# Kernel tuning notes

Measured on AMD Instinct MI355X. Metric: run time of the kernel, lower is better.

Reference implementation:

```python
import jax, jax.numpy as jnp
import numpy as np

B, H, W = 16, 512, 512
N_BINS = 511          # round(mean(shape)) - 1 for (512, 512)
MAX_R = 1.0           # (1 + min(shape)/max(shape)) / 2 for square image


def _bin_ids():
    # Precompute per-pixel radial shell index (replaces the list of boolean shell masks).
    frame = max(H, W)
    xx, yy = np.mgrid[:H, :W]
    ellipse = ((xx - H / 2) * 2 / frame) ** 2 + ((yy - W / 2) * 2 / frame) ** 2
    r2 = np.linspace(0.0, MAX_R, N_BINS + 1)[1:] ** 2
    # shell k = { r2[k-1] <= ellipse < r2[k] }; pixels with ellipse >= r2[-1] map to
    # overflow bin N_BINS and are dropped, exactly matching the xor'd ellipse masks.
    return jnp.asarray(np.searchsorted(r2, ellipse.ravel(), side='right').astype(np.int32))


BIN_IDS = _bin_ids()  # [H*W] int32 in [0, N_BINS]


def setup_inputs() -> dict:
    key = jax.random.key(0)
    k1, k2 = jax.random.split(key)
    return {
        "z_": jax.random.normal(k1, (B, H, W, 2), dtype=jnp.float32),
        "t_": jax.random.normal(k2, (B, H, W, 2), dtype=jnp.float32),
    }


def _shell_sums(x):
    # x: [B, H*W] -> per-shell sums [B, N_BINS+1] in a single fused segment-sum pass.
    return jax.vmap(lambda v: jax.ops.segment_sum(v, BIN_IDS, num_segments=N_BINS + 1))(x)


def reference(z_, t_):
    tc = t_[..., 0] + 1j * t_[..., 1]          # [B,H,W] complex target
    zc = z_[..., 0] + 1j * z_[..., 1]
    Ft = jnp.fft.fft2(tc, axes=(-2, -1))
    Fe = jnp.fft.fft2(zc - tc, axes=(-2, -1))
    norm_coeff = Ft.real ** 2 + Ft.imag ** 2   # |FFT(target)|^2, [B,H,W]
    errors = Fe.real ** 2 + Fe.imag ** 2       # |FFT(z - target)|^2
    es = _shell_sums(errors.reshape(B, -1))[:, :N_BINS]      # drop overflow bin
    ns = _shell_sums(norm_coeff.reshape(B, -1))[:, :N_BINS]
    nre = es / jnp.maximum(ns, 1e-8)           # per-batch, per-shell normed error
    # per_shell_loss = per-batch sum over shells; loss = mean over batch
    return jnp.mean(jnp.sum(nre, axis=1))
```

## Files before the change

### kernel.cpp

```cpp
#include <hip/hip_runtime.h>

#define HH 512
#define WW 512
#define NBATCH 16
#define NBINS 512

#define PI_F 3.14159265358979323846f

#define SW(r) ((r) ^ (((r) >> 4) & 0xF))
#define TSW(c, hh) (((c) << 3) + ((hh) ^ (((c) >> 1) & 7)))

#define DPP_SHR(x, n) __builtin_amdgcn_update_dpp(0, (x), 0x110 + (n), 0xF, 0xF, true)
#define DPP_SHL1(x)   __builtin_amdgcn_update_dpp(0, (x), 0x101,       0xF, 0xF, true)

__device__ __forceinline__ float2 cadd(float2 a, float2 b){ return make_float2(a.x+b.x, a.y+b.y); }
__device__ __forceinline__ float2 csub(float2 a, float2 b){ return make_float2(a.x-b.x, a.y-b.y); }
__device__ __forceinline__ float2 cmul(float2 a, float2 b){
    return make_float2(a.x*b.x - a.y*b.y, a.x*b.y + a.y*b.x);
}

__device__ __forceinline__ void dft8(const float2* a, float2* y) {
    const float s2 = 0.70710678118654752440f;
    float2 t02a = cadd(a[0], a[4]), t02s = csub(a[0], a[4]);
    float2 t13a = cadd(a[2], a[6]), t13s = csub(a[2], a[6]);
    float2 E0 = cadd(t02a, t13a);
    float2 E2 = csub(t02a, t13a);
    float2 E1 = make_float2(t02s.x + t13s.y, t02s.y - t13s.x);
    float2 E3 = make_float2(t02s.x - t13s.y, t02s.y + t13s.x);
    float2 u02a = cadd(a[1], a[5]), u02s = csub(a[1], a[5]);
    float2 u13a = cadd(a[3], a[7]), u13s = csub(a[3], a[7]);
    float2 O0 = cadd(u02a, u13a);
    float2 O2 = csub(u02a, u13a);
    float2 O1 = make_float2(u02s.x + u13s.y, u02s.y - u13s.x);
    float2 O3 = make_float2(u02s.x - u13s.y, u02s.y + u13s.x);
    float2 wO1 = make_float2(s2 * (O1.x + O1.y), s2 * (O1.y - O1.x));
    float2 wO2 = make_float2(O2.y, -O2.x);
    float2 wO3 = make_float2(s2 * (O3.y - O3.x), -s2 * (O3.x + O3.y));
    y[0] = cadd(E0, O0);  y[4] = csub(E0, O0);
    y[1] = cadd(E1, wO1); y[5] = csub(E1, wO1);
    y[2] = cadd(E2, wO2); y[6] = csub(E2, wO2);
    y[3] = cadd(E3, wO3); y[7] = csub(E3, wO3);
}

__device__ __forceinline__ void twiddle8(float base, float2* w) {
    float s1, c1, s4, c4;
    __sincosf(base, &s1, &c1);
    __sincosf(4.0f * base, &s4, &c4);
    w[0] = make_float2(1.0f, 0.0f);
    w[1] = make_float2(c1, s1);
    w[2] = cmul(w[1], w[1]);
    w[3] = cmul(w[2], w[1]);
    w[4] = make_float2(c4, s4);
    w[5] = cmul(w[4], w[1]);
    w[6] = cmul(w[4], w[2]);
    w[7] = cmul(w[4], w[3]);
}

__device__ __forceinline__ void fft512_stage0_store(float2* rb, int lane, const float2* a) {
    float2 y[8]; dft8(a, y);
    float2 w[8]; twiddle8(-PI_F * (float)lane * (1.0f / 256.0f), w);
#pragma unroll
    for (int r = 0; r < 8; ++r) rb[SW(8 * lane + r)] = cmul(y[r], w[r]);
}

__device__ __forceinline__ void fft512_stage1(float2* rb, int lane) {
    float2 a[8];
#pragma unroll
    for (int u = 0; u < 8; ++u) a[u] = rb[SW(lane + 64 * u)];
    float2 y[8]; dft8(a, y);
    float2 w[8]; twiddle8(-PI_F * (float)(lane >> 3) * (1.0f / 32.0f), w);
    const int qb = (lane & 7) + ((lane >> 3) << 6);
#pragma unroll
    for (int r = 0; r < 8; ++r) rb[SW(qb + 8 * r)] = cmul(y[r], w[r]);
}

__device__ __forceinline__ void fft512_stage2(const float2* rb, int lane, float2* y) {
    float2 a[8];
#pragma unroll
    for (int u = 0; u < 8; ++u) a[u] = rb[SW(lane + 64 * u)];
    dft8(a, y);
}

__global__ __launch_bounds__(512, 4)
void row_fft_kernel(const float2* __restrict__ z, const float2* __restrict__ t,
                    float2* __restrict__ fieldsT, int b0) {
    __shared__ float2 buf[8 * 512];
    const int tid  = threadIdx.x;
    const int lane = tid & 63;
    const int g    = tid >> 6;
    const int bid  = blockIdx.x;
    const int hg   = bid & 63;
    const int lb   = bid >> 6;
    const int b    = b0 + lb;
    const int h    = (hg << 3) | g;
    const size_t rowOff = ((size_t)(b * HH + h)) * WW;

    const float2* tr = t + rowOff;
    const float2* zr = z + rowOff;
    float2 tv[8], zv[8];
#pragma unroll
    for (int u = 0; u < 8; ++u) tv[u] = tr[lane + 64 * u];
#pragma unroll
    for (int u = 0; u < 8; ++u) zv[u] = zr[lane + 64 * u];

    float2* rb = buf + (g << 9);
#pragma unroll
    for (int f = 0; f < 2; ++f) {
        float2 a[8];
        if (f == 0) {
#pragma unroll
            for (int u = 0; u < 8; ++u) a[u] = tv[u];
        } else {
#pragma unroll
            for (int u = 0; u < 8; ++u) a[u] = make_float2(zv[u].x - tv[u].x,
                                                           zv[u].y - tv[u].y);
        }
        fft512_stage0_store(rb, lane, a);
        __builtin_amdgcn_wave_barrier();
        fft512_stage1(rb, lane);
        __builtin_amdgcn_wave_barrier();
        float2 y[8];
        fft512_stage2(rb, lane, y);

        __syncthreads();
#pragma unroll
        for (int r = 0; r < 8; ++r) {
            int c = lane + (r << 6);
            buf[TSW(c, g)] = y[r];
        }
        __syncthreads();
        float2* outF = fieldsT + ((size_t)(lb * 2 + f) << 18);
#pragma unroll
        for (int k = 0; k < 8; ++k) {
            int e  = tid + (k << 9);
            int c  = e >> 3;
            int hh = e & 7;
            outF[((size_t)c << 9) + (hg << 3) + hh] = buf[TSW(c, hh)];
        }
        __syncthreads();
    }
}

__global__ __launch_bounds__(512, 4)
void col_fft_bin_kernel(const float2* __restrict__ fieldsT,
                        float* __restrict__ partials, int b0) {
    __shared__ float2 buf[8 * 512];
    const int tid  = threadIdx.x;
    const int lane = tid & 63;
    const int g    = tid >> 6;
    const int bid  = blockIdx.x;
    const int cg   = bid & 63;
    const int fl   = bid >> 6;
    const int f    = fl & 1;
    const int b    = b0 + (fl >> 1);
    const int c    = (cg << 3) | g;

    const float2* colT = fieldsT + (((size_t)fl << 9) + c) * 512;
    float2 a[8];
#pragma unroll
    for (int u = 0; u < 8; ++u) a[u] = colT[lane + (u << 6)];

    float2* rb = buf + (g << 9);
    fft512_stage0_store(rb, lane, a);
    __builtin_amdgcn_wave_barrier();
    fft512_stage1(rb, lane);
    __builtin_amdgcn_wave_barrier();
    float2 y[8];
    fft512_stage2(rb, lane, y);
    __builtin_amdgcn_wave_barrier();
    __asm__ volatile("" ::: "memory");

#pragma unroll
    for (int j = 0; j < 4; ++j) rb[lane + (j << 6)] = make_float2(0.0f, 0.0f);
    __builtin_amdgcn_wave_barrier();
    __asm__ volatile("" ::: "memory");

    float* histw = (float*)rb;
    const int dc = c - 256;
    const unsigned fc2i = (unsigned)(dc * dc);
    const int l15 = lane & 15;
#pragma unroll
    for (int r = 0; r < 8; ++r) {
        int k  = lane + (r << 6);
        int dk = k - 256;
        unsigned m = (unsigned)(dk * dk) + fc2i;
        int bin = (int)(sqrtf((float)m) * (511.0f / 256.0f));
        unsigned long long rhs = 261121ull * (unsigned long long)m;
        unsigned bp1 = (unsigned)(bin + 1);
        if (((unsigned long long)(bp1 * bp1) << 16) <= rhs) ++bin;
        else if (((unsigned long long)((unsigned)bin * (unsigned)bin) << 16) > rhs) --bin;
        bin = (m < 65536u) ? bin : 511;

        float v = y[r].x * y[r].x + y[r].y * y[r].y;

        int nb; float nv;
        nb = DPP_SHR(bin, 1);
        nv = __int_as_float(DPP_SHR(__float_as_int(v), 1));
        v += (l15 >= 1 && nb == bin) ? nv : 0.0f;
        nb = DPP_SHR(bin, 2);
        nv = __int_as_float(DPP_SHR(__float_as_int(v), 2));
        v += (l15 >= 2 && nb == bin) ? nv : 0.0f;
        nb = DPP_SHR(bin, 4);
        nv = __int_as_float(DPP_SHR(__float_as_int(v), 4));
        v += (l15 >= 4 && nb == bin) ? nv : 0.0f;
        nb = DPP_SHR(bin, 8);
        nv = __int_as_float(DPP_SHR(__float_as_int(v), 8));
        v += (l15 >= 8 && nb == bin) ? nv : 0.0f;

        int nxt = DPP_SHL1(bin);
        if (l15 == 15 || nxt != bin)
            atomicAdd(&histw[bin], v);
    }
    __syncthreads();

    float s = 0.0f;
    const float* bufF = (const float*)buf;
#pragma unroll
    for (int gg = 0; gg < 8; ++gg) s += bufF[(gg << 10) + tid];
    partials[(((size_t)cg << 5) + (size_t)(f * NBATCH + b)) * NBINS + tid] = s;
}

__global__ __launch_bounds__(512)
void reduce_bins_kernel(const float* __restrict__ partials, float* __restrict__ bins) {
    __shared__ float red[512];
    const int tid = threadIdx.x;
    const int fl  = blockIdx.x >> 2;
    const int q   = blockIdx.x & 3;
    const int bin = (q << 7) + (tid & 127);
    const int ch  = tid >> 7;
    float s = 0.0f;
#pragma unroll
    for (int j = 0; j < 16; ++j) {
        int cg = (ch << 4) + j;
        s += partials[((size_t)(cg << 5) + fl) * NBINS + bin];
    }
    red[tid] = s;
    __syncthreads();
    if (tid < 128) {
        bins[(size_t)fl * NBINS + bin] =
            red[tid] + red[tid + 128] + red[tid + 256] + red[tid + 384];
    }
}

__global__ __launch_bounds__(512)
void loss_kernel(const float* __restrict__ bins, float* __restrict__ outp) {
    __shared__ float red[512];
    const int tid = threadIdx.x;
    float acc = 0.0f;
    if (tid < 511) {
#pragma unroll 4
        for (int b = 0; b < NBATCH; ++b) {
            float ns = bins[((size_t)b) * NBINS + tid];
            float es = bins[((size_t)(NBATCH + b)) * NBINS + tid];
            acc += es / fmaxf(ns, 1e-8f);
        }
    }
    red[tid] = acc;
    __syncthreads();
    for (int s = 256; s > 0; s >>= 1) {
        if (tid < s) red[tid] += red[tid + s];
        __syncthreads();
    }
    if (tid == 0) outp[0] = red[0] * (1.0f / NBATCH);
}

extern "C" void kernel_launch(void* const* d_in, const int* in_sizes, int n_in,
                              void* d_out, int out_size, void* d_ws, size_t ws_size,
                              hipStream_t stream) {
    const float2* z = (const float2*)d_in[0];
    const float2* t = (const float2*)d_in[1];
    float* outp = (float*)d_out;

    const size_t partialsBytes = 64ull * 2 * NBATCH * NBINS * sizeof(float);
    const size_t binsBytes     = (size_t)2 * NBATCH * NBINS * sizeof(float);
    const size_t fixedBytes    = partialsBytes + binsBytes;
    const size_t fpb = (size_t)2 * HH * WW * sizeof(float2);

    int CB = 16;
    while (CB > 1 && fixedBytes + (size_t)CB * fpb > ws_size) CB >>= 1;

    float*  partials = (float*)d_ws;
    float*  bins     = (float*)((char*)d_ws + partialsBytes);
    float2* fieldsT  = (float2*)((char*)d_ws + fixedBytes);

    for (int b0 = 0; b0 < NBATCH; b0 += CB) {
        row_fft_kernel<<<CB * 64, 512, 0, stream>>>(z, t, fieldsT, b0);
        col_fft_bin_kernel<<<CB * 2 * 64, 512, 0, stream>>>(fieldsT, partials, b0);
    }
    reduce_bins_kernel<<<128, 512, 0, stream>>>(partials, bins);
    loss_kernel<<<1, 512, 0, stream>>>(bins, outp);
}
```

Measured before the change: 157.6 us.

## Shrink column-FFT blocks to 256 threads and reduce bins via replicated global atomics

Column FFT blocks now cover 4 columns with 256 threads instead of 8 with 512, which halves shared memory per block and allows more blocks per CU. Per-block histograms are no longer written to a 64-way partials array. They are atomically added into 8 replicated bin arrays, so the reduce kernel only sums 8 copies. This adds a memset and global atomic contention in exchange for less partial-write traffic and a lighter reduction.

New measurement: 160.2 us. No clear change (+1.7%).

```diff
diff --git a/kernel.cpp b/kernel.cpp
--- a/kernel.cpp
+++ b/kernel.cpp
@@ -4,6 +4,7 @@
 #define WW 512
 #define NBATCH 16
 #define NBINS 512
+#define NREP 8
 
 #define PI_F 3.14159265358979323846f
 
@@ -141,21 +142,21 @@
     }
 }
 
-__global__ __launch_bounds__(512, 4)
+__global__ __launch_bounds__(256, 8)
 void col_fft_bin_kernel(const float2* __restrict__ fieldsT,
-                        float* __restrict__ partials, int b0) {
-    __shared__ float2 buf[8 * 512];
+                        float* __restrict__ binsR, int b0) {
+    __shared__ float2 buf[4 * 512];
     const int tid  = threadIdx.x;
     const int lane = tid & 63;
     const int g    = tid >> 6;
     const int bid  = blockIdx.x;
-    const int cg   = bid & 63;
-    const int fl   = bid >> 6;
-    const int f    = fl & 1;
-    const int b    = b0 + (fl >> 1);
-    const int c    = (cg << 3) | g;
-
-    const float2* colT = fieldsT + (((size_t)fl << 9) + c) * 512;
+    const int cq   = bid & 127;
+    const int f    = (bid >> 7) & 1;
+    const int lb   = bid >> 8;
+    const int b    = b0 + lb;
+    const int c    = (cq << 2) | g;
+
+    const float2* colT = fieldsT + (((size_t)(lb * 2 + f) << 9) + c) * 512;
     float2 a[8];
 #pragma unroll
     for (int u = 0; u < 8; ++u) a[u] = colT[lane + (u << 6)];
@@ -213,33 +214,28 @@
     }
     __syncthreads();
 
+    const float* bufF = (const float*)buf;
+    float s0 = 0.0f, s1 = 0.0f;
+#pragma unroll
+    for (int w = 0; w < 4; ++w) {
+        s0 += bufF[(w << 10) + tid];
+        s1 += bufF[(w << 10) + 256 + tid];
+    }
+    const int fl = f * NBATCH + b;
+    float* dst = binsR + ((size_t)(bid & (NREP - 1)) * 2 * NBATCH + fl) * NBINS;
+    atomicAdd(&dst[tid], s0);
+    atomicAdd(&dst[tid + 256], s1);
+}
+
+__global__ __launch_bounds__(512)
+void reduce_bins_kernel(const float* __restrict__ binsR, float* __restrict__ bins) {
+    const int tid = threadIdx.x;
+    const int fl  = blockIdx.x;
     float s = 0.0f;
-    const float* bufF = (const float*)buf;
-#pragma unroll
-    for (int gg = 0; gg < 8; ++gg) s += bufF[(gg << 10) + tid];
-    partials[(((size_t)cg << 5) + (size_t)(f * NBATCH + b)) * NBINS + tid] = s;
-}
-
-__global__ __launch_bounds__(512)
-void reduce_bins_kernel(const float* __restrict__ partials, float* __restrict__ bins) {
-    __shared__ float red[512];
-    const int tid = threadIdx.x;
-    const int fl  = blockIdx.x >> 2;
-    const int q   = blockIdx.x & 3;
-    const int bin = (q << 7) + (tid & 127);
-    const int ch  = tid >> 7;
-    float s = 0.0f;
-#pragma unroll
-    for (int j = 0; j < 16; ++j) {
-        int cg = (ch << 4) + j;
-        s += partials[((size_t)(cg << 5) + fl) * NBINS + bin];
-    }
-    red[tid] = s;
-    __syncthreads();
-    if (tid < 128) {
-        bins[(size_t)fl * NBINS + bin] =
-            red[tid] + red[tid + 128] + red[tid + 256] + red[tid + 384];
-    }
+#pragma unroll
+    for (int x = 0; x < NREP; ++x)
+        s += binsR[((size_t)x * 2 * NBATCH + fl) * NBINS + tid];
+    bins[(size_t)fl * NBINS + tid] = s;
 }
 
 __global__ __launch_bounds__(512)
@@ -271,22 +267,24 @@
     const float2* t = (const float2*)d_in[1];
     float* outp = (float*)d_out;
 
-    const size_t partialsBytes = 64ull * 2 * NBATCH * NBINS * sizeof(float);
-    const size_t binsBytes     = (size_t)2 * NBATCH * NBINS * sizeof(float);
-    const size_t fixedBytes    = partialsBytes + binsBytes;
+    const size_t binsRBytes = (size_t)NREP * 2 * NBATCH * NBINS * sizeof(float);
+    const size_t binsBytes  = (size_t)2 * NBATCH * NBINS * sizeof(float);
+    const size_t fixedBytes = binsRBytes + binsBytes;
     const size_t fpb = (size_t)2 * HH * WW * sizeof(float2);
 
     int CB = 16;
     while (CB > 1 && fixedBytes + (size_t)CB * fpb > ws_size) CB >>= 1;
 
-    float*  partials = (float*)d_ws;
-    float*  bins     = (float*)((char*)d_ws + partialsBytes);
-    float2* fieldsT  = (float2*)((char*)d_ws + fixedBytes);
+    float*  binsR   = (float*)d_ws;
+    float*  bins    = (float*)((char*)d_ws + binsRBytes);
+    float2* fieldsT = (float2*)((char*)d_ws + fixedBytes);
+
+    hipMemsetAsync(binsR, 0, binsRBytes, stream);
 
     for (int b0 = 0; b0 < NBATCH; b0 += CB) {
         row_fft_kernel<<<CB * 64, 512, 0, stream>>>(z, t, fieldsT, b0);
-        col_fft_bin_kernel<<<CB * 2 * 64, 512, 0, stream>>>(fieldsT, partials, b0);
-    }
-    reduce_bins_kernel<<<128, 512, 0, stream>>>(partials, bins);
+        col_fft_bin_kernel<<<CB * 2 * 128, 256, 0, stream>>>(fieldsT, binsR, b0);
+    }
+    reduce_bins_kernel<<<32, 512, 0, stream>>>(binsR, bins);
     loss_kernel<<<1, 512, 0, stream>>>(bins, outp);
 }
```

## Software-pipeline row and column FFT chunks in a fused double-buffered kernel

Applied to the files above, without the earlier changes.

Merges the row-FFT and column-FFT/binning kernels into one launch that runs row work for batch chunk k alongside column work for chunk k-1, using two ping-pong intermediate buffers. Blocks are interleaved one row block to two column blocks so both phases share the GPU at once. The intermediate layout also changes so each pair of adjacent columns is stored interleaved, which turns the row kernel's transposed writes into 16-byte pairs. The goal is to overlap the memory-bound row phase with the column phase and cut launch tail effects, at the cost of smaller chunks, more launches and strided 8-byte column loads.

Measured after the change: 174.6 us. 1.11x slower.

```diff
diff --git a/kernel.cpp b/kernel.cpp
--- a/kernel.cpp
+++ b/kernel.cpp
@@ -4,6 +4,7 @@
 #define WW 512
 #define NBATCH 16
 #define NBINS 512
+#define NCG 64
 
 #define PI_F 3.14159265358979323846f
 
@@ -81,16 +82,16 @@
     dft8(a, y);
 }
 
-__global__ __launch_bounds__(512, 4)
-void row_fft_kernel(const float2* __restrict__ z, const float2* __restrict__ t,
-                    float2* __restrict__ fieldsT, int b0) {
-    __shared__ float2 buf[8 * 512];
+__device__ __forceinline__ void row_body(float2* buf,
+                                         const float2* __restrict__ z,
+                                         const float2* __restrict__ t,
+                                         float2* __restrict__ fieldsT,
+                                         int b0, int rbid) {
     const int tid  = threadIdx.x;
     const int lane = tid & 63;
     const int g    = tid >> 6;
-    const int bid  = blockIdx.x;
-    const int hg   = bid & 63;
-    const int lb   = bid >> 6;
+    const int hg   = rbid & 63;
+    const int lb   = rbid >> 6;
     const int b    = b0 + lb;
     const int h    = (hg << 3) | g;
     const size_t rowOff = ((size_t)(b * HH + h)) * WW;
@@ -135,30 +136,31 @@
             int e  = tid + (k << 9);
             int c  = e >> 3;
             int hh = e & 7;
-            outF[((size_t)c << 9) + (hg << 3) + hh] = buf[TSW(c, hh)];
+            int hr = (hg << 3) | hh;
+            outF[((size_t)(c >> 1) << 10) + (hr << 1) + (c & 1)] = buf[TSW(c, hh)];
         }
         __syncthreads();
     }
 }
 
-__global__ __launch_bounds__(512, 4)
-void col_fft_bin_kernel(const float2* __restrict__ fieldsT,
-                        float* __restrict__ partials, int b0) {
-    __shared__ float2 buf[8 * 512];
+__device__ __forceinline__ void col_body(float2* buf,
+                                         const float2* __restrict__ fieldsT,
+                                         float* __restrict__ partials,
+                                         int b0, int cbid) {
     const int tid  = threadIdx.x;
     const int lane = tid & 63;
     const int g    = tid >> 6;
-    const int bid  = blockIdx.x;
-    const int cg   = bid & 63;
-    const int fl   = bid >> 6;
-    const int f    = fl & 1;
-    const int b    = b0 + (fl >> 1);
+    const int cg   = cbid & (NCG - 1);
+    const int f    = (cbid >> 6) & 1;
+    const int lb   = cbid >> 7;
+    const int b    = b0 + lb;
     const int c    = (cg << 3) | g;
 
-    const float2* colT = fieldsT + (((size_t)fl << 9) + c) * 512;
+    const float2* colT = fieldsT + ((size_t)(lb * 2 + f) << 18)
+                                 + ((size_t)(c >> 1) << 10) + (c & 1);
     float2 a[8];
 #pragma unroll
-    for (int u = 0; u < 8; ++u) a[u] = colT[lane + (u << 6)];
+    for (int u = 0; u < 8; ++u) a[u] = colT[(lane + (u << 6)) << 1];
 
     float2* rb = buf + (g << 9);
     fft512_stage0_store(rb, lane, a);
@@ -217,7 +219,27 @@
     const float* bufF = (const float*)buf;
 #pragma unroll
     for (int gg = 0; gg < 8; ++gg) s += bufF[(gg << 10) + tid];
-    partials[(((size_t)cg << 5) + (size_t)(f * NBATCH + b)) * NBINS + tid] = s;
+    const int fl = f * NBATCH + b;
+    partials[(((size_t)cg << 5) + (size_t)fl) * NBINS + tid] = s;
+}
+
+__global__ __launch_bounds__(512, 4)
+void fused_kernel(const float2* __restrict__ z, const float2* __restrict__ t,
+                  float2* __restrict__ wbuf, const float2* __restrict__ rbuf,
+                  float* __restrict__ partials,
+                  int rowB0, int colB0, int nRow, int nCol) {
+    __shared__ float2 buf[8 * 512];
+    const int bid = blockIdx.x;
+    if (nRow > 0 && nCol > 0) {
+        const int q = bid / 3;
+        const int r = bid - 3 * q;
+        if (r == 0) row_body(buf, z, t, wbuf, rowB0, q);
+        else        col_body(buf, rbuf, partials, colB0, 2 * q + (r - 1));
+    } else if (nRow > 0) {
+        row_body(buf, z, t, wbuf, rowB0, bid);
+    } else {
+        col_body(buf, rbuf, partials, colB0, bid);
+    }
 }
 
 __global__ __launch_bounds__(512)
@@ -271,21 +293,28 @@
     const float2* t = (const float2*)d_in[1];
     float* outp = (float*)d_out;
 
-    const size_t partialsBytes = 64ull * 2 * NBATCH * NBINS * sizeof(float);
+    const size_t partialsBytes = (size_t)NCG * 2 * NBATCH * NBINS * sizeof(float);
     const size_t binsBytes     = (size_t)2 * NBATCH * NBINS * sizeof(float);
     const size_t fixedBytes    = partialsBytes + binsBytes;
     const size_t fpb = (size_t)2 * HH * WW * sizeof(float2);
 
-    int CB = 16;
-    while (CB > 1 && fixedBytes + (size_t)CB * fpb > ws_size) CB >>= 1;
+    int CH = 4;
+    while (CH > 1 && fixedBytes + (size_t)2 * CH * fpb > ws_size) CH >>= 1;
 
     float*  partials = (float*)d_ws;
     float*  bins     = (float*)((char*)d_ws + partialsBytes);
-    float2* fieldsT  = (float2*)((char*)d_ws + fixedBytes);
-
-    for (int b0 = 0; b0 < NBATCH; b0 += CB) {
-        row_fft_kernel<<<CB * 64, 512, 0, stream>>>(z, t, fieldsT, b0);
-        col_fft_bin_kernel<<<CB * 2 * 64, 512, 0, stream>>>(fieldsT, partials, b0);
+    float2* bufA     = (float2*)((char*)d_ws + fixedBytes);
+    float2* bufB     = bufA + (size_t)CH * 2 * HH * WW;
+
+    const int nch = NBATCH / CH;
+    for (int k = 0; k <= nch; ++k) {
+        const int nRow = (k < nch) ? CH * 64 : 0;
+        const int nCol = (k > 0) ? CH * 2 * NCG : 0;
+        float2* wbuf = (k & 1) ? bufB : bufA;
+        const float2* rbuf = (k > 0) ? (((k - 1) & 1) ? bufB : bufA) : bufA;
+        fused_kernel<<<nRow + nCol, 512, 0, stream>>>(z, t, wbuf, rbuf, partials,
+                                                      k * CH, (k - 1) * CH,
+                                                      nRow, nCol);
     }
     reduce_bins_kernel<<<128, 512, 0, stream>>>(partials, bins);
     loss_kernel<<<1, 512, 0, stream>>>(bins, outp);
```
